# Performance work log

Measured on AMD Instinct MI355X. Metric: run time of the kernel, lower is better.

## Reference

```python
import jax, jax.numpy as jnp
import numpy as np
from jax import lax

R = 7                      # pooler_resolution
SCALES = (0.25, 0.125, 0.0625, 0.03125)
SCORE_THRESH = 0.05        # args.roi_test_score_thresh
NMS_THRESH = 0.5           # args.roi_nms_thresh
TOPK = 100                 # args.roi_nms_topk_post
SCALE_CLAMP = float(np.log(1000.0 / 16))


def _pool_level(f, boxes, scale):
    # f: [C,H,W]; boxes: [M,4] in image coords. RoIPool approximated by
    # nearest-neighbor sample at each of the 7x7 bin centers.
    C, H, W = f.shape
    b = boxes * scale
    x1, y1, x2, y2 = b[:, 0], b[:, 1], b[:, 2], b[:, 3]
    bw = jnp.maximum(x2 - x1, 1.0) / R
    bh = jnp.maximum(y2 - y1, 1.0) / R
    cs = jnp.arange(R, dtype=b.dtype) + 0.5
    gx = x1[:, None] + cs * bw[:, None]          # [M,R]
    gy = y1[:, None] + cs * bh[:, None]          # [M,R]
    ix = jnp.clip(gx.astype(jnp.int32), 0, W - 1)
    iy = jnp.clip(gy.astype(jnp.int32), 0, H - 1)
    fh = jnp.transpose(f, (1, 2, 0))             # [H,W,C]
    out = fh[iy[:, :, None], ix[:, None, :]]     # [M,R,R,C]
    return jnp.transpose(out, (0, 3, 1, 2))      # [M,C,R,R]


def _assign_levels(boxes):
    # detectron2-style FPN level assignment: canonical level 4 at size 224
    w = boxes[:, 2] - boxes[:, 0]
    h = boxes[:, 3] - boxes[:, 1]
    s = jnp.sqrt(jnp.maximum(w * h, 1e-6))
    lvl = jnp.floor(4.0 + jnp.log2(s / 224.0 + 1e-8))
    return jnp.clip(lvl, 2, 5).astype(jnp.int32) - 2   # index into p2..p5


def _pool_image(f2, f3, f4, f5, boxes):
    pooled = jnp.stack([_pool_level(f, boxes, s)
                        for f, s in zip((f2, f3, f4, f5), SCALES)])  # [4,M,C,R,R]
    idx = _assign_levels(boxes)
    return pooled[idx, jnp.arange(boxes.shape[0])]     # [M,C,R,R]


def _apply_deltas(boxes, deltas):
    w = boxes[:, 2] - boxes[:, 0]
    h = boxes[:, 3] - boxes[:, 1]
    cx = boxes[:, 0] + 0.5 * w
    cy = boxes[:, 1] + 0.5 * h
    dx, dy = deltas[:, 0], deltas[:, 1]
    dw = jnp.minimum(deltas[:, 2], SCALE_CLAMP)
    dh = jnp.minimum(deltas[:, 3], SCALE_CLAMP)
    pcx = dx * w + cx
    pcy = dy * h + cy
    pw = jnp.exp(dw) * w
    ph = jnp.exp(dh) * h
    return jnp.stack([pcx - 0.5 * pw, pcy - 0.5 * ph,
                      pcx + 0.5 * pw, pcy + 0.5 * ph], axis=1)


def _pairwise_iou(a, b):
    area_a = (a[:, 2] - a[:, 0]) * (a[:, 3] - a[:, 1])
    area_b = (b[:, 2] - b[:, 0]) * (b[:, 3] - b[:, 1])
    lt = jnp.maximum(a[:, None, :2], b[None, :, :2])
    rb = jnp.minimum(a[:, None, 2:], b[None, :, 2:])
    wh = jnp.clip(rb - lt, 0.0)
    inter = wh[..., 0] * wh[..., 1]
    return inter / jnp.maximum(area_a[:, None] + area_b[None, :] - inter, 1e-9)


def _nms_image(boxes, scores, hw):
    # boxes [M,4], scores [M], hw = (H,W) float
    H, W = hw[0], hw[1]
    boxes = jnp.stack([jnp.clip(boxes[:, 0], 0.0, W),
                       jnp.clip(boxes[:, 1], 0.0, H),
                       jnp.clip(boxes[:, 2], 0.0, W),
                       jnp.clip(boxes[:, 3], 0.0, H)], axis=1)
    order = jnp.argsort(-scores)
    b = boxes[order]
    s = scores[order]
    M = b.shape[0]
    keep0 = s > SCORE_THRESH
    iou = _pairwise_iou(b, b)
    idx = jnp.arange(M)

    def body(i, keep):
        suppress = (iou[i] > NMS_THRESH) & (idx > i) & keep[i]
        return keep & ~suppress

    keep = lax.fori_loop(0, M, body, keep0)
    keep = keep & (jnp.cumsum(keep.astype(jnp.int32)) <= TOPK)
    return b, s, keep, order


def setup_inputs() -> dict:
    key = jax.random.key(0)
    ks = jax.random.split(key, 12)
    N, M, C = 2, 1000, 256
    H, W = 800, 1216
    fc_in, fc_dim = C * R * R, 1024
    p2 = jax.random.normal(ks[0], (N, C, H // 4, W // 4), jnp.float32)
    p3 = jax.random.normal(ks[1], (N, C, H // 8, W // 8), jnp.float32)
    p4 = jax.random.normal(ks[2], (N, C, H // 16, W // 16), jnp.float32)
    p5 = jax.random.normal(ks[3], (N, C, H // 32, W // 32), jnp.float32)
    u = jax.random.uniform(ks[4], (N, M, 4))
    cx = u[..., 0] * (W - 1)
    cy = u[..., 1] * (H - 1)
    bw = 16.0 + u[..., 2] * 480.0
    bh = 16.0 + u[..., 3] * 480.0
    x1 = jnp.clip(cx - 0.5 * bw, 0.0, W - 8.0)
    y1 = jnp.clip(cy - 0.5 * bh, 0.0, H - 8.0)
    x2 = jnp.clip(cx + 0.5 * bw, x1 + 4.0, float(W))
    y2 = jnp.clip(cy + 0.5 * bh, y1 + 4.0, float(H))
    proposals = jnp.stack([x1, y1, x2, y2], axis=-1)
    image_sizes = jnp.array([[H, W], [H, W]], dtype=jnp.int32)
    return {
        'p2': p2, 'p3': p3, 'p4': p4, 'p5': p5,
        'proposals': proposals, 'image_sizes': image_sizes,
        'W1': jax.random.normal(ks[5], (fc_in, fc_dim), jnp.float32) * 0.01,
        'b1': jnp.zeros((fc_dim,), jnp.float32),
        'W2': jax.random.normal(ks[6], (fc_dim, fc_dim), jnp.float32) * 0.01,
        'b2': jnp.zeros((fc_dim,), jnp.float32),
        'Wc': jax.random.normal(ks[7], (fc_dim, 2), jnp.float32) * 0.01,
        'bc': jnp.zeros((2,), jnp.float32),
        'Wb': jax.random.normal(ks[8], (fc_dim, 4), jnp.float32) * 0.001,
        'bb': jnp.zeros((4,), jnp.float32),
    }


def reference(p2, p3, p4, p5, proposals, image_sizes,
              W1, b1, W2, b2, Wc, bc, Wb, bb):
    N, M, _ = proposals.shape
    pooled = jax.vmap(_pool_image)(p2, p3, p4, p5, proposals)  # [N,M,C,R,R]
    x = pooled.reshape(N * M, -1)
    x = jax.nn.relu(x @ W1 + b1)
    x = jax.nn.relu(x @ W2 + b2)
    cls_score = x @ Wc + bc                                    # [NM,2]
    deltas = x @ Wb + bb                                       # [NM,4]
    scores = jax.nn.softmax(cls_score, axis=1)[:, 1].reshape(N, M)
    pred_boxes = _apply_deltas(proposals.reshape(-1, 4), deltas).reshape(N, M, 4)
    boxes_s, scores_s, keep, order = jax.vmap(_nms_image)(
        pred_boxes, scores, image_sizes.astype(jnp.float32))
    return boxes_s, scores_s, keep, order
```

## Files before the change

### kernel.cpp

```cpp
#include <hip/hip_runtime.h>
#include <math.h>

#define NBOX 1000
#define NIMG 2
#define CCH 256
#define FCIN 12544
#define FCD 1024
#define TOPK 100
#define SCALE_CLAMP_F ((float)4.135166556742356)
#define KC 384
#define NPANEL 33
#define RB 16
#define NGROUP 125
#define CHUNK 128
#define RB2 8
#define NP2 3
#define R1 8
#define HB 8

__global__ void prep_kernel(const float* __restrict__ props, int* __restrict__ prep) {
    int b = blockIdx.x * blockDim.x + threadIdx.x;
    if (b >= NIMG * NBOX) return;
    int n = b / NBOX;
    const float* pr = props + (size_t)b * 4;
    float x1 = pr[0], y1 = pr[1], x2 = pr[2], y2 = pr[3];

    float w = __fsub_rn(x2, x1), h = __fsub_rn(y2, y1);
    float s = sqrtf(fmaxf(__fmul_rn(w, h), 1e-6f));
    float l2 = (float)log2((double)__fadd_rn(__fdiv_rn(s, 224.0f), 1e-8f));
    float lv = floorf(__fadd_rn(4.0f, l2));
    lv = fminf(fmaxf(lv, 2.0f), 5.0f);
    int lvl = (int)lv - 2;

    int H, W; float scale;
    if (lvl == 0)      { H = 200; W = 304; scale = 0.25f; }
    else if (lvl == 1) { H = 100; W = 152; scale = 0.125f; }
    else if (lvl == 2) { H = 50;  W = 76;  scale = 0.0625f; }
    else               { H = 25;  W = 38;  scale = 0.03125f; }

    float xs1 = __fmul_rn(x1, scale), ys1 = __fmul_rn(y1, scale);
    float xs2 = __fmul_rn(x2, scale), ys2 = __fmul_rn(y2, scale);
    float bw = __fdiv_rn(fmaxf(__fsub_rn(xs2, xs1), 1.0f), 7.0f);
    float bh = __fdiv_rn(fmaxf(__fsub_rn(ys2, ys1), 1.0f), 7.0f);

    int* pb = prep + b * 20;
    pb[0] = lvl;
    pb[1] = n * CCH * H * W;
    pb[2] = H * W;
#pragma unroll
    for (int i = 0; i < 7; i++) {
        float cs = (float)i + 0.5f;
        float gx = __fadd_rn(xs1, __fmul_rn(cs, bw));
        float gy = __fadd_rn(ys1, __fmul_rn(cs, bh));
        int vx = (int)gx;
        int vy = (int)gy;
        vx = vx < 0 ? 0 : (vx > W - 1 ? W - 1 : vx);
        vy = vy < 0 ? 0 : (vy > H - 1 ? H - 1 : vy);
        pb[4 + i] = vx;
        pb[12 + i] = vy * W;
    }
}

#define FMASTEP(KB, WV)                                               \
    {                                                                 \
        const float4* xv = (const float4*)&xs[(KB)][0];               \
        float4 a0 = xv[0], a1 = xv[1], a2 = xv[2], a3 = xv[3];        \
        float xr[16] = {a0.x, a0.y, a0.z, a0.w, a1.x, a1.y, a1.z, a1.w, \
                        a2.x, a2.y, a2.z, a2.w, a3.x, a3.y, a3.z, a3.w}; \
        _Pragma("unroll")                                             \
        for (int r = 0; r < RB; r++) {                                \
            acc[r][0] = fmaf(xr[r], WV.x, acc[r][0]);                 \
            acc[r][1] = fmaf(xr[r], WV.y, acc[r][1]);                 \
            acc[r][2] = fmaf(xr[r], WV.z, acc[r][2]);                 \
            acc[r][3] = fmaf(xr[r], WV.w, acc[r][3]);                 \
        }                                                             \
    }

__global__ __launch_bounds__(256, 4) void fc1_panel(
    const float* __restrict__ p2, const float* __restrict__ p3,
    const float* __restrict__ p4, const float* __restrict__ p5,
    const int* __restrict__ prep, const float* __restrict__ W1,
    float* __restrict__ part, int g0, int gs) {
    __shared__ float xs[CHUNK][RB];
    __shared__ int s_ix[RB][7], s_iyW[RB][7], s_HW[RB];
    __shared__ const float* s_fp[RB];

    int tid = threadIdx.x;
    int gy = blockIdx.x;
    int p = blockIdx.y;
    int row0 = (g0 + gy) * RB;
    int k0 = p * KC;
    int kt = (p == NPANEL - 1) ? 256 : KC;

    if (tid < RB) {
        const int* pb = prep + (row0 + tid) * 20;
        int lvl = pb[0];
        s_fp[tid] = (lvl == 0 ? p2 : lvl == 1 ? p3 : lvl == 2 ? p4 : p5) + pb[1];
        s_HW[tid] = pb[2];
#pragma unroll
        for (int j = 0; j < 7; j++) { s_ix[tid][j] = pb[4 + j]; s_iyW[tid][j] = pb[12 + j]; }
    }
    __syncthreads();

    float acc[RB][4];
#pragma unroll
    for (int r = 0; r < RB; r++)
#pragma unroll
        for (int j = 0; j < 4; j++) acc[r][j] = 0.0f;

    const float* wp = W1 + (size_t)k0 * FCD + tid * 4;

    for (int ck = 0; ck < kt; ck += CHUNK) {
        for (int e = tid; e < CHUNK * RB; e += 256) {
            int kk = e >> 4;
            int r = e & 15;
            int k = k0 + ck + kk;
            int c = k / 49;
            int pp = k - c * 49;
            int gyy = pp / 7;
            int gxx = pp - gyy * 7;
            xs[kk][r] = s_fp[r][c * s_HW[r] + s_iyW[r][gyy] + s_ix[r][gxx]];
        }
        __syncthreads();

        const float* wc = wp + (size_t)ck * FCD;
        float4 wA = *(const float4*)wc;
        for (int kk = 0; kk < CHUNK; kk += 2) {
            float4 wB = *(const float4*)(wc + (size_t)(kk + 1) * FCD);
            FMASTEP(kk, wA)
            if (kk + 2 < CHUNK) wA = *(const float4*)(wc + (size_t)(kk + 2) * FCD);
            FMASTEP(kk + 1, wB)
        }
        __syncthreads();
    }

    size_t pstride = (size_t)gs * RB * FCD;
    float* po = part + (size_t)p * pstride + ((size_t)gy * RB) * FCD + tid * 4;
#pragma unroll
    for (int r = 0; r < RB; r++) {
        float4 v = make_float4(acc[r][0], acc[r][1], acc[r][2], acc[r][3]);
        *(float4*)(po + (size_t)r * FCD) = v;
    }
}

__global__ __launch_bounds__(256, 4) void fc2_panel(
    const float* __restrict__ X1, const float* __restrict__ W2,
    float* __restrict__ part) {
    __shared__ float xs2[CHUNK][RB2];
    int tid = threadIdx.x;
    int gy = blockIdx.x;
    int p = blockIdx.y;
    int row0 = gy * RB2;
    int k0 = p * KC;
    int kt = (p == NP2 - 1) ? 256 : KC;

    float acc[RB2][4];
#pragma unroll
    for (int r = 0; r < RB2; r++)
#pragma unroll
        for (int j = 0; j < 4; j++) acc[r][j] = 0.0f;

    const float* wp = W2 + (size_t)k0 * FCD + tid * 4;

    for (int ck = 0; ck < kt; ck += CHUNK) {
        for (int e = tid; e < CHUNK * RB2; e += 256) {
            int kk = e >> 3;
            int r = e & 7;
            xs2[kk][r] = X1[(size_t)(row0 + r) * FCD + k0 + ck + kk];
        }
        __syncthreads();

        const float* wc = wp + (size_t)ck * FCD;
        float4 wA = *(const float4*)wc;
        for (int kk = 0; kk < CHUNK; kk += 2) {
            float4 wB = *(const float4*)(wc + (size_t)(kk + 1) * FCD);
            {
                const float4* xv = (const float4*)&xs2[kk][0];
                float4 a0 = xv[0], a1 = xv[1];
                float xr[8] = {a0.x, a0.y, a0.z, a0.w, a1.x, a1.y, a1.z, a1.w};
#pragma unroll
                for (int r = 0; r < RB2; r++) {
                    acc[r][0] = fmaf(xr[r], wA.x, acc[r][0]);
                    acc[r][1] = fmaf(xr[r], wA.y, acc[r][1]);
                    acc[r][2] = fmaf(xr[r], wA.z, acc[r][2]);
                    acc[r][3] = fmaf(xr[r], wA.w, acc[r][3]);
                }
            }
            if (kk + 2 < CHUNK) wA = *(const float4*)(wc + (size_t)(kk + 2) * FCD);
            {
                const float4* xv = (const float4*)&xs2[kk + 1][0];
                float4 a0 = xv[0], a1 = xv[1];
                float xr[8] = {a0.x, a0.y, a0.z, a0.w, a1.x, a1.y, a1.z, a1.w};
#pragma unroll
                for (int r = 0; r < RB2; r++) {
                    acc[r][0] = fmaf(xr[r], wB.x, acc[r][0]);
                    acc[r][1] = fmaf(xr[r], wB.y, acc[r][1]);
                    acc[r][2] = fmaf(xr[r], wB.z, acc[r][2]);
                    acc[r][3] = fmaf(xr[r], wB.w, acc[r][3]);
                }
            }
        }
        __syncthreads();
    }

    size_t pstride = (size_t)NIMG * NBOX * FCD;
    float* po = part + (size_t)p * pstride + ((size_t)row0) * FCD + tid * 4;
#pragma unroll
    for (int r = 0; r < RB2; r++) {
        float4 v = make_float4(acc[r][0], acc[r][1], acc[r][2], acc[r][3]);
        *(float4*)(po + (size_t)r * FCD) = v;
    }
}

__global__ void fold_bias_relu(const float* __restrict__ part, const float* __restrict__ bias,
                               float* __restrict__ Xout, int row_base, int rows_s, int npanel) {
    int idx = blockIdx.x * 256 + threadIdx.x;
    if (idx >= rows_s * FCD) return;
    size_t stride = (size_t)rows_s * FCD;
    float tot = part[idx];
    for (int p = 1; p < npanel; p++)
        tot = __fadd_rn(tot, part[(size_t)p * stride + idx]);
    int c = idx & (FCD - 1);
    float v = __fadd_rn(tot, bias[c]);
    Xout[(size_t)row_base * FCD + idx] = fmaxf(v, 0.0f);
}

#define FMA8(BUF, KB)                                                                   \
    _Pragma("unroll")                                                                   \
    for (int u = 0; u < 8; u++) {                                                       \
        const float4* xv = (const float4*)&xs[(KB) + u][0];                             \
        float4 a0 = xv[0], a1 = xv[1];                                                  \
        float wx = BUF[u].x, wy = BUF[u].y;                                             \
        acc[0][0] = fmaf(a0.x, wx, acc[0][0]); acc[0][1] = fmaf(a0.x, wy, acc[0][1]);   \
        acc[1][0] = fmaf(a0.y, wx, acc[1][0]); acc[1][1] = fmaf(a0.y, wy, acc[1][1]);   \
        acc[2][0] = fmaf(a0.z, wx, acc[2][0]); acc[2][1] = fmaf(a0.z, wy, acc[2][1]);   \
        acc[3][0] = fmaf(a0.w, wx, acc[3][0]); acc[3][1] = fmaf(a0.w, wy, acc[3][1]);   \
        acc[4][0] = fmaf(a1.x, wx, acc[4][0]); acc[4][1] = fmaf(a1.x, wy, acc[4][1]);   \
        acc[5][0] = fmaf(a1.y, wx, acc[5][0]); acc[5][1] = fmaf(a1.y, wy, acc[5][1]);   \
        acc[6][0] = fmaf(a1.z, wx, acc[6][0]); acc[6][1] = fmaf(a1.z, wy, acc[6][1]);   \
        acc[7][0] = fmaf(a1.w, wx, acc[7][0]); acc[7][1] = fmaf(a1.w, wy, acc[7][1]);   \
    }

template <int KT>
__device__ __forceinline__ void fc_panel2(const float* __restrict__ wp,
                                          const float (*xs)[R1],
                                          float acc[R1][2]) {
    float2 wa[8], wb[8];
#pragma unroll
    for (int u = 0; u < 8; u++) wa[u] = *(const float2*)(wp + (size_t)u * FCD);
    for (int kk = 0; kk < KT; kk += 16) {
#pragma unroll
        for (int u = 0; u < 8; u++)
            wb[u] = *(const float2*)(wp + (size_t)(kk + 8 + u) * FCD);
        FMA8(wa, kk)
        if (kk + 16 < KT) {
#pragma unroll
            for (int u = 0; u < 8; u++)
                wa[u] = *(const float2*)(wp + (size_t)(kk + 16 + u) * FCD);
        }
        FMA8(wb, kk + 8)
    }
}

__global__ __launch_bounds__(256) void fc1_fallback(
    const float* __restrict__ p2, const float* __restrict__ p3,
    const float* __restrict__ p4, const float* __restrict__ p5,
    const int* __restrict__ prep, const float* __restrict__ W1,
    const float* __restrict__ b1, float* __restrict__ X1) {
    __shared__ float xs[KC][R1];
    __shared__ int s_ix[R1][7], s_iyW[R1][7], s_HW[R1];
    __shared__ const float* s_fp[R1];

    int tid = threadIdx.x;
    int c0 = blockIdx.x * 512 + tid * 2;
    int row0 = blockIdx.y * R1;

    if (tid < R1) {
        const int* pb = prep + (row0 + tid) * 20;
        int lvl = pb[0];
        s_fp[tid] = (lvl == 0 ? p2 : lvl == 1 ? p3 : lvl == 2 ? p4 : p5) + pb[1];
        s_HW[tid] = pb[2];
#pragma unroll
        for (int j = 0; j < 7; j++) { s_ix[tid][j] = pb[4 + j]; s_iyW[tid][j] = pb[12 + j]; }
    }

    float tot[R1][2];
#pragma unroll
    for (int r = 0; r < R1; r++) { tot[r][0] = 0.0f; tot[r][1] = 0.0f; }

    for (int k0 = 0; k0 < FCIN; k0 += KC) {
        int kt = FCIN - k0; if (kt > KC) kt = KC;
        __syncthreads();
        for (int e = tid; e < kt * R1; e += 256) {
            int kk = e >> 3;
            int r = e & 7;
            int k = k0 + kk;
            int c = k / 49;
            int p = k - c * 49;
            int gy = p / 7;
            int gx = p - gy * 7;
            xs[kk][r] = s_fp[r][c * s_HW[r] + s_iyW[r][gy] + s_ix[r][gx]];
        }
        __syncthreads();

        float acc[R1][2];
#pragma unroll
        for (int r = 0; r < R1; r++) { acc[r][0] = 0.0f; acc[r][1] = 0.0f; }

        const float* wp = W1 + (size_t)k0 * FCD + c0;
        if (kt == KC) fc_panel2<KC>(wp, xs, acc);
        else          fc_panel2<256>(wp, xs, acc);

#pragma unroll
        for (int r = 0; r < R1; r++) {
            tot[r][0] = __fadd_rn(tot[r][0], acc[r][0]);
            tot[r][1] = __fadd_rn(tot[r][1], acc[r][1]);
        }
    }
    float bv0 = b1[c0], bv1 = b1[c0 + 1];
#pragma unroll
    for (int r = 0; r < R1; r++) {
        float v0 = __fadd_rn(tot[r][0], bv0);
        float v1 = __fadd_rn(tot[r][1], bv1);
        X1[(size_t)(row0 + r) * FCD + c0]     = fmaxf(v0, 0.0f);
        X1[(size_t)(row0 + r) * FCD + c0 + 1] = fmaxf(v1, 0.0f);
    }
}

__global__ __launch_bounds__(256) void fc2_seq(
    const float* __restrict__ X1, const float* __restrict__ W2,
    const float* __restrict__ b2, float* __restrict__ X2) {
    __shared__ float xs[KC][R1];
    int tid = threadIdx.x;
    int c0 = blockIdx.x * 512 + tid * 2;
    int row0 = blockIdx.y * R1;

    float tot[R1][2];
#pragma unroll
    for (int r = 0; r < R1; r++) { tot[r][0] = 0.0f; tot[r][1] = 0.0f; }

    for (int k0 = 0; k0 < FCD; k0 += KC) {
        int kt = FCD - k0; if (kt > KC) kt = KC;
        __syncthreads();
        for (int e = tid; e < kt * R1; e += 256) {
            int kk = e >> 3;
            int r = e & 7;
            xs[kk][r] = X1[(size_t)(row0 + r) * FCD + k0 + kk];
        }
        __syncthreads();

        float acc[R1][2];
#pragma unroll
        for (int r = 0; r < R1; r++) { acc[r][0] = 0.0f; acc[r][1] = 0.0f; }

        const float* wp = W2 + (size_t)k0 * FCD + c0;
        if (kt == KC) fc_panel2<KC>(wp, xs, acc);
        else          fc_panel2<256>(wp, xs, acc);

#pragma unroll
        for (int r = 0; r < R1; r++) {
            tot[r][0] = __fadd_rn(tot[r][0], acc[r][0]);
            tot[r][1] = __fadd_rn(tot[r][1], acc[r][1]);
        }
    }
    float bv0 = b2[c0], bv1 = b2[c0 + 1];
#pragma unroll
    for (int r = 0; r < R1; r++) {
        float v0 = __fadd_rn(tot[r][0], bv0);
        float v1 = __fadd_rn(tot[r][1], bv1);
        X2[(size_t)(row0 + r) * FCD + c0]     = fmaxf(v0, 0.0f);
        X2[(size_t)(row0 + r) * FCD + c0 + 1] = fmaxf(v1, 0.0f);
    }
}

__global__ __launch_bounds__(256) void heads_par(
    const float* __restrict__ X2,
    const float* __restrict__ Wc, const float* __restrict__ bc,
    const float* __restrict__ Wb, const float* __restrict__ bb_,
    const float* __restrict__ props, const int* __restrict__ img_sz,
    float* __restrict__ SC, float* __restrict__ BX) {
    int tid = threadIdx.x;
    int b0 = blockIdx.x * HB;
    __shared__ float xsh[HB][FCD];
    __shared__ float wsh[6][FCD];
    __shared__ float red[HB][6][3];
    __shared__ float lg[HB][6];

    for (int e = tid; e < HB * FCD; e += 256) {
        int r = e >> 10, k = e & (FCD - 1);
        xsh[r][k] = X2[(size_t)(b0 + r) * FCD + k];
    }
    for (int e = tid; e < 6 * FCD; e += 256) {
        int q = e / FCD, k = e - q * FCD;
        wsh[q][k] = (q < 2) ? Wc[k * 2 + q] : Wb[k * 4 + (q - 2)];
    }
    __syncthreads();

    int c = tid & 31, r = tid >> 5;
    if (c < 18) {
        int q = c / 3, p = c - q * 3;
        int k0 = p * KC;
        int kt = (p == 2) ? 256 : KC;
        float acc = 0.0f;
        for (int k = k0; k < k0 + kt; k++)
            acc = fmaf(xsh[r][k], wsh[q][k], acc);
        red[r][q][p] = acc;
    }
    __syncthreads();

    if (c < 6) {
        int q = c;
        float t = __fadd_rn(__fadd_rn(red[r][q][0], red[r][q][1]), red[r][q][2]);
        float bias = (q < 2) ? bc[q] : bb_[q - 2];
        lg[r][q] = __fadd_rn(t, bias);
    }
    __syncthreads();

    if (c == 0) {
        int b = b0 + r;
        float c0 = lg[r][0], c1 = lg[r][1];
        float mx = fmaxf(c0, c1);
        float e0 = (float)exp((double)__fsub_rn(c0, mx));
        float e1 = (float)exp((double)__fsub_rn(c1, mx));
        SC[b] = __fdiv_rn(e1, __fadd_rn(e0, e1));

        int n = b / NBOX;
        const float* pr = props + (size_t)b * 4;
        float x1 = pr[0], y1 = pr[1], x2 = pr[2], y2 = pr[3];
        float w = __fsub_rn(x2, x1), h = __fsub_rn(y2, y1);
        float cx = __fadd_rn(x1, __fmul_rn(0.5f, w));
        float cy = __fadd_rn(y1, __fmul_rn(0.5f, h));
        float dx = lg[r][2], dy = lg[r][3];
        float dw = fminf(lg[r][4], SCALE_CLAMP_F);
        float dh = fminf(lg[r][5], SCALE_CLAMP_F);
        float pcx = __fadd_rn(__fmul_rn(dx, w), cx);
        float pcy = __fadd_rn(__fmul_rn(dy, h), cy);
        float pw = __fmul_rn((float)exp((double)dw), w);
        float ph = __fmul_rn((float)exp((double)dh), h);
        float bx1 = __fsub_rn(pcx, __fmul_rn(0.5f, pw));
        float by1 = __fsub_rn(pcy, __fmul_rn(0.5f, ph));
        float bx2 = __fadd_rn(pcx, __fmul_rn(0.5f, pw));
        float by2 = __fadd_rn(pcy, __fmul_rn(0.5f, ph));
        float Hf = (float)img_sz[n * 2 + 0], Wf = (float)img_sz[n * 2 + 1];
        bx1 = fminf(fmaxf(bx1, 0.0f), Wf);
        by1 = fminf(fmaxf(by1, 0.0f), Hf);
        bx2 = fminf(fmaxf(bx2, 0.0f), Wf);
        by2 = fminf(fmaxf(by2, 0.0f), Hf);
        BX[(size_t)b * 4 + 0] = bx1;
        BX[(size_t)b * 4 + 1] = by1;
        BX[(size_t)b * 4 + 2] = bx2;
        BX[(size_t)b * 4 + 3] = by2;
    }
}

__global__ __launch_bounds__(1024) void nms_kernel(const float* __restrict__ SC,
                                                   const float* __restrict__ BX,
                                                   float* __restrict__ out) {
    int n = blockIdx.x;
    __shared__ float sraw[NBOX];
    __shared__ float ssort[NBOX];
    __shared__ float bsort[NBOX][4];
    __shared__ int ord[NBOX];
    __shared__ unsigned char keep[NBOX];
    int tid = threadIdx.x;

    for (int j = tid; j < NBOX; j += 1024) sraw[j] = SC[n * NBOX + j];
    __syncthreads();

    if (tid < NBOX) {
        float sj = sraw[tid];
        int r = 0;
        for (int k = 0; k < NBOX; k++) {
            float sk = sraw[k];
            r += (sk > sj) || (sk == sj && k < tid);
        }
        ord[r] = tid;
        ssort[r] = sj;
#pragma unroll
        for (int k = 0; k < 4; k++) bsort[r][k] = BX[((size_t)n * NBOX + tid) * 4 + k];
        keep[r] = (sj > 0.05f) ? 1 : 0;
    }
    __syncthreads();

    for (int i = 0; i < NBOX - 1; i++) {
        if (keep[i] && tid > i && tid < NBOX && keep[tid]) {
            float ax1 = bsort[i][0], ay1 = bsort[i][1], ax2 = bsort[i][2], ay2 = bsort[i][3];
            float bx1 = bsort[tid][0], by1 = bsort[tid][1], bx2 = bsort[tid][2], by2 = bsort[tid][3];
            float areaA = __fmul_rn(__fsub_rn(ax2, ax1), __fsub_rn(ay2, ay1));
            float areaB = __fmul_rn(__fsub_rn(bx2, bx1), __fsub_rn(by2, by1));
            float ix1 = fmaxf(ax1, bx1), iy1 = fmaxf(ay1, by1);
            float ix2 = fminf(ax2, bx2), iy2 = fminf(ay2, by2);
            float iw = fmaxf(__fsub_rn(ix2, ix1), 0.0f);
            float ih = fmaxf(__fsub_rn(iy2, iy1), 0.0f);
            float inter = __fmul_rn(iw, ih);
            float denom = fmaxf(__fsub_rn(__fadd_rn(areaA, areaB), inter), 1e-9f);
            if (__fdiv_rn(inter, denom) > 0.5f) keep[tid] = 0;
        }
        __syncthreads();
    }

    if (tid == 0) {
        int c = 0;
        for (int r = 0; r < NBOX; r++) {
            int k = keep[r];
            c += k;
            keep[r] = (k && (c <= TOPK)) ? 1 : 0;
        }
    }
    __syncthreads();

    float* boxes_o = out;
    float* scores_o = out + (size_t)NIMG * NBOX * 4;
    float* keep_o = scores_o + (size_t)NIMG * NBOX;
    float* ord_o = keep_o + (size_t)NIMG * NBOX;
    for (int r = tid; r < NBOX; r += 1024) {
#pragma unroll
        for (int k = 0; k < 4; k++)
            boxes_o[((size_t)n * NBOX + r) * 4 + k] = bsort[r][k];
        scores_o[n * NBOX + r] = ssort[r];
        keep_o[n * NBOX + r] = (float)keep[r];
        ord_o[n * NBOX + r] = (float)ord[r];
    }
}

extern "C" void kernel_launch(void* const* d_in, const int* in_sizes, int n_in,
                              void* d_out, int out_size, void* d_ws, size_t ws_size,
                              hipStream_t stream) {
    const float* p2 = (const float*)d_in[0];
    const float* p3 = (const float*)d_in[1];
    const float* p4 = (const float*)d_in[2];
    const float* p5 = (const float*)d_in[3];
    const float* props = (const float*)d_in[4];
    const int* img = (const int*)d_in[5];
    const float* W1 = (const float*)d_in[6];
    const float* b1 = (const float*)d_in[7];
    const float* W2 = (const float*)d_in[8];
    const float* b2 = (const float*)d_in[9];
    const float* Wc = (const float*)d_in[10];
    const float* bc = (const float*)d_in[11];
    const float* Wb = (const float*)d_in[12];
    const float* bb = (const float*)d_in[13];

    float* X1 = (float*)d_ws;
    float* X2 = X1 + (size_t)2000 * FCD;
    float* SCf = X2 + (size_t)2000 * FCD;
    float* BXf = SCf + 2000;
    int* prep = (int*)(BXf + 8000);
    float* part = (float*)(prep + 2000 * 20);
    size_t used = (size_t)((char*)part - (char*)d_ws);
    size_t avail = ws_size > used ? ws_size - used : 0;

    prep_kernel<<<(NIMG * NBOX + 255) / 256, 256, 0, stream>>>(props, prep);

    int gmax = 0;
    const int cand[4] = {125, 63, 32, 16};
    for (int i = 0; i < 4; i++) {
        size_t need = (size_t)NPANEL * cand[i] * RB * FCD * sizeof(float);
        if (need <= avail) { gmax = cand[i]; break; }
    }

    if (gmax > 0) {
        for (int g0 = 0; g0 < NGROUP; g0 += gmax) {
            int gs = NGROUP - g0; if (gs > gmax) gs = gmax;
            dim3 gA(gs, NPANEL);
            fc1_panel<<<gA, 256, 0, stream>>>(p2, p3, p4, p5, prep, W1, part, g0, gs);
            int nelem = gs * RB * FCD;
            fold_bias_relu<<<(nelem + 255) / 256, 256, 0, stream>>>(part, b1, X1,
                                                                    g0 * RB, gs * RB, NPANEL);
        }
    } else {
        dim3 gfc(2, (NIMG * NBOX) / R1);
        fc1_fallback<<<gfc, 256, 0, stream>>>(p2, p3, p4, p5, prep, W1, b1, X1);
    }

    size_t need2 = (size_t)NP2 * NIMG * NBOX * FCD * sizeof(float);
    if (need2 <= avail) {
        dim3 g2(NIMG * NBOX / RB2, NP2);
        fc2_panel<<<g2, 256, 0, stream>>>(X1, W2, part);
        int nelem2 = NIMG * NBOX * FCD;
        fold_bias_relu<<<(nelem2 + 255) / 256, 256, 0, stream>>>(part, b2, X2,
                                                                 0, NIMG * NBOX, NP2);
    } else {
        dim3 gfc2(2, (NIMG * NBOX) / R1);
        fc2_seq<<<gfc2, 256, 0, stream>>>(X1, W2, b2, X2);
    }

    heads_par<<<NIMG * NBOX / HB, 256, 0, stream>>>(X2, Wc, bc, Wb, bb, props, img, SCf, BXf);

    nms_kernel<<<NIMG, 1024, 0, stream>>>(SCf, BXf, (float*)d_out);
}
```

Measured before the change: 1.162 ms.

## Replace sequential barrier-per-box NMS with bitmask IoU matrix and single-wave scan

The NMS kernel used to loop over 999 sorted boxes with a block-wide barrier after each step. Now every thread computes a 64-bit suppression mask of IoU > 0.5 against all later boxes, storing it in dynamic LDS. One wavefront then scans the masks serially using shuffles, and top-K keep flags come from popcount prefix sums. This removes about a thousand __syncthreads, at the cost of a full IoU triangle and roughly 156KB of dynamic LDS per block, which is close to the per-CU limit.

```diff
diff --git a/kernel.cpp b/kernel.cpp
--- a/kernel.cpp
+++ b/kernel.cpp
@@ -17,6 +17,7 @@
 #define NP2 3
 #define R1 8
 #define HB 8
+#define NW 16
 
 __global__ void prep_kernel(const float* __restrict__ props, int* __restrict__ prep) {
     int b = blockIdx.x * blockDim.x + threadIdx.x;
@@ -453,15 +454,19 @@
     }
 }
 
-__global__ __launch_bounds__(1024) void nms_kernel(const float* __restrict__ SC,
-                                                   const float* __restrict__ BX,
-                                                   float* __restrict__ out) {
+__global__ __launch_bounds__(1024) void nms_bitmask(const float* __restrict__ SC,
+                                                    const float* __restrict__ BX,
+                                                    float* __restrict__ out) {
+    extern __shared__ unsigned long long dsm[];
+    unsigned long long* mask = dsm;
+    unsigned long long* kmask = dsm + NW * NBOX;
+    unsigned int* pref = (unsigned int*)(kmask + NW);
+    float* sraw = (float*)(pref + NW);
+    float* ssort = sraw + NBOX;
+    float* bs = ssort + NBOX;
+    int* ord = (int*)(bs + NBOX * 4);
+
     int n = blockIdx.x;
-    __shared__ float sraw[NBOX];
-    __shared__ float ssort[NBOX];
-    __shared__ float bsort[NBOX][4];
-    __shared__ int ord[NBOX];
-    __shared__ unsigned char keep[NBOX];
     int tid = threadIdx.x;
 
     for (int j = tid; j < NBOX; j += 1024) sraw[j] = SC[n * NBOX + j];
@@ -477,35 +482,62 @@
         ord[r] = tid;
         ssort[r] = sj;
 #pragma unroll
-        for (int k = 0; k < 4; k++) bsort[r][k] = BX[((size_t)n * NBOX + tid) * 4 + k];
-        keep[r] = (sj > 0.05f) ? 1 : 0;
-    }
-    __syncthreads();
-
-    for (int i = 0; i < NBOX - 1; i++) {
-        if (keep[i] && tid > i && tid < NBOX && keep[tid]) {
-            float ax1 = bsort[i][0], ay1 = bsort[i][1], ax2 = bsort[i][2], ay2 = bsort[i][3];
-            float bx1 = bsort[tid][0], by1 = bsort[tid][1], bx2 = bsort[tid][2], by2 = bsort[tid][3];
-            float areaA = __fmul_rn(__fsub_rn(ax2, ax1), __fsub_rn(ay2, ay1));
-            float areaB = __fmul_rn(__fsub_rn(bx2, bx1), __fsub_rn(by2, by1));
-            float ix1 = fmaxf(ax1, bx1), iy1 = fmaxf(ay1, by1);
-            float ix2 = fminf(ax2, bx2), iy2 = fminf(ay2, by2);
-            float iw = fmaxf(__fsub_rn(ix2, ix1), 0.0f);
-            float ih = fmaxf(__fsub_rn(iy2, iy1), 0.0f);
-            float inter = __fmul_rn(iw, ih);
-            float denom = fmaxf(__fsub_rn(__fadd_rn(areaA, areaB), inter), 1e-9f);
-            if (__fdiv_rn(inter, denom) > 0.5f) keep[tid] = 0;
-        }
-        __syncthreads();
-    }
+        for (int k = 0; k < 4; k++) bs[r * 4 + k] = BX[((size_t)n * NBOX + tid) * 4 + k];
+    }
+    __syncthreads();
+
+    if (tid < NW) {
+        unsigned long long m = 0;
+        for (int b = 0; b < 64; b++) {
+            int r = tid * 64 + b;
+            if (r < NBOX && ssort[r] > 0.05f) m |= 1ull << b;
+        }
+        kmask[tid] = m;
+    }
+
+    if (tid < NBOX) {
+        int i = tid;
+        float ax1 = bs[i * 4 + 0], ay1 = bs[i * 4 + 1], ax2 = bs[i * 4 + 2], ay2 = bs[i * 4 + 3];
+        float areaA = __fmul_rn(__fsub_rn(ax2, ax1), __fsub_rn(ay2, ay1));
+        for (int w = 0; w < NW; w++) {
+            unsigned long long m = 0;
+            int jbase = w * 64;
+            for (int b = 0; b < 64; b++) {
+                int j = jbase + b;
+                if (j < NBOX && j > i) {
+                    float bx1 = bs[j * 4 + 0], by1 = bs[j * 4 + 1];
+                    float bx2 = bs[j * 4 + 2], by2 = bs[j * 4 + 3];
+                    float areaB = __fmul_rn(__fsub_rn(bx2, bx1), __fsub_rn(by2, by1));
+                    float ix1 = fmaxf(ax1, bx1), iy1 = fmaxf(ay1, by1);
+                    float ix2 = fminf(ax2, bx2), iy2 = fminf(ay2, by2);
+                    float iw = fmaxf(__fsub_rn(ix2, ix1), 0.0f);
+                    float ih = fmaxf(__fsub_rn(iy2, iy1), 0.0f);
+                    float inter = __fmul_rn(iw, ih);
+                    float denom = fmaxf(__fsub_rn(__fadd_rn(areaA, areaB), inter), 1e-9f);
+                    if (__fdiv_rn(inter, denom) > 0.5f) m |= 1ull << b;
+                }
+            }
+            mask[(size_t)w * NBOX + i] = m;
+        }
+    }
+    __syncthreads();
+
+    if (tid < 64) {
+        int lane = tid;
+        unsigned long long myw = (lane < NW) ? kmask[lane] : 0ull;
+        for (int i = 0; i < NBOX; i++) {
+            unsigned long long cw = __shfl(myw, i >> 6);
+            if ((cw >> (i & 63)) & 1ull) {
+                if (lane < NW) myw &= ~mask[(size_t)lane * NBOX + i];
+            }
+        }
+        if (lane < NW) kmask[lane] = myw;
+    }
+    __syncthreads();
 
     if (tid == 0) {
-        int c = 0;
-        for (int r = 0; r < NBOX; r++) {
-            int k = keep[r];
-            c += k;
-            keep[r] = (k && (c <= TOPK)) ? 1 : 0;
-        }
+        unsigned int c = 0;
+        for (int w = 0; w < NW; w++) { pref[w] = c; c += (unsigned int)__popcll(kmask[w]); }
     }
     __syncthreads();
 
@@ -513,12 +545,19 @@
     float* scores_o = out + (size_t)NIMG * NBOX * 4;
     float* keep_o = scores_o + (size_t)NIMG * NBOX;
     float* ord_o = keep_o + (size_t)NIMG * NBOX;
-    for (int r = tid; r < NBOX; r += 1024) {
+    if (tid < NBOX) {
+        int r = tid;
+        int w = r >> 6, b = r & 63;
+        unsigned long long kw = kmask[w];
+        int bit = (int)((kw >> b) & 1ull);
+        unsigned long long lowmask = b ? ((1ull << b) - 1ull) : 0ull;
+        int csum = (int)pref[w] + (int)__popcll(kw & lowmask) + bit;
+        int kfin = (bit && csum <= TOPK) ? 1 : 0;
 #pragma unroll
         for (int k = 0; k < 4; k++)
-            boxes_o[((size_t)n * NBOX + r) * 4 + k] = bsort[r][k];
+            boxes_o[((size_t)n * NBOX + r) * 4 + k] = bs[r * 4 + k];
         scores_o[n * NBOX + r] = ssort[r];
-        keep_o[n * NBOX + r] = (float)keep[r];
+        keep_o[n * NBOX + r] = (float)kfin;
         ord_o[n * NBOX + r] = (float)ord[r];
     }
 }
@@ -587,5 +626,7 @@
 
     heads_par<<<NIMG * NBOX / HB, 256, 0, stream>>>(X2, Wc, bc, Wb, bb, props, img, SCf, BXf);
 
-    nms_kernel<<<NIMG, 1024, 0, stream>>>(SCf, BXf, (float*)d_out);
-}
+    size_t nms_lds = (size_t)NW * NBOX * 8 + NW * 8 + NW * 4
+                   + (size_t)(NBOX + NBOX + NBOX * 4) * 4 + NBOX * 4;
+    nms_bitmask<<<NIMG, 1024, nms_lds, stream>>>(SCf, BXf, (float*)d_out);
+}
```

New measurement: 1.115 ms. 4.1% less time.
